# Kernel tuning notes

Hardware: AMD Instinct MI355X
Metric: run time of the kernel (lower is better)

Reference implementation:

```python
import jax, jax.numpy as jnp
import numpy as np

N = 50000   # nodes (subjects in population graph)
E = 800000  # edges (similarity graph, avg degree 16)
F = 128     # node features


def setup_inputs() -> dict:
    key = jax.random.key(0)
    ks = jax.random.split(key, 8)

    def glorot(k, shape):
        scale = 1.0 / np.sqrt(shape[0])
        return jax.random.normal(k, shape, jnp.float32) * scale

    x = jax.random.normal(ks[0], (N, F), jnp.float32)
    edge_index = jax.random.randint(ks[1], (2, E), 0, N, dtype=jnp.int64)
    return {
        "x": x,
        "edge_index": edge_index,
        "W1": glorot(ks[2], (F, 128)),   "b1": jnp.zeros((128,), jnp.float32),
        "W2": glorot(ks[3], (128, 64)),  "b2": jnp.zeros((64,), jnp.float32),
        "Wf1": glorot(ks[4], (64, 32)),  "bf1": jnp.zeros((32,), jnp.float32),
        "Wf2": glorot(ks[5], (32, 1)),   "bf2": jnp.zeros((1,), jnp.float32),
    }


def reference(x, edge_index, W1, b1, W2, b2, Wf1, bf1, Wf2, bf2):
    n = x.shape[0]
    # GCNConv (PyG default): add self-loops, symmetric deg^{-1/2} normalization
    loops = jnp.arange(n, dtype=edge_index.dtype)
    src = jnp.concatenate([edge_index[0], loops])  # [E+N]
    dst = jnp.concatenate([edge_index[1], loops])  # [E+N]
    deg = jax.ops.segment_sum(jnp.ones_like(dst, x.dtype), dst, num_segments=n)
    dinv = deg ** -0.5  # deg >= 1 thanks to self-loops
    norm = (dinv[src] * dinv[dst])[:, None]  # [E+N, 1]

    def gcn_conv(h, W, b):
        h = h @ W                                    # transform [n, out]
        msg = h[src] * norm                          # gather + normalize
        agg = jax.ops.segment_sum(msg, dst, num_segments=n)  # scatter-add
        return agg + b

    h = jnp.tanh(gcn_conv(x, W1, b1))
    h = jnp.tanh(gcn_conv(h, W2, b2))
    h = jnp.tanh(h @ Wf1 + bf1)
    return h @ Wf2 + bf2  # [n, 1] brain-age prediction
```

## Files before the change

kernel.cpp:

```cpp
#include <hip/hip_runtime.h>
#include <hip/hip_fp16.h>
#include <math.h>

#define TPB 256
#define CAP 64
#define BSHIFT 7
#define BSPAN 128
#define NBLK 256

typedef int   nt_i4 __attribute__((ext_vector_type(4)));
typedef unsigned nt_u4 __attribute__((ext_vector_type(4)));
typedef unsigned nt_u2 __attribute__((ext_vector_type(2)));

__global__ __launch_bounds__(TPB) void detect_dtype(const int* __restrict__ e,
                                                    int* __restrict__ flag) {
  __shared__ int found;
  if (threadIdx.x == 0) found = 0;
  __syncthreads();
  int nz = 0;
  for (int i = threadIdx.x; i < 2048; i += TPB)
    nz |= (e[2 * i + 1] != 0) ? 1 : 0;
  if (nz) atomicOr(&found, 1);
  __syncthreads();
  if (threadIdx.x == 0) *flag = found;
}

__device__ __forceinline__ void load_edge(const void* eptr, int flag, int E,
                                          int e, int& s, int& d) {
  if (flag) {
    const int* p = (const int*)eptr;
    s = p[e];
    d = p[E + e];
  } else {
    const long long* p = (const long long*)eptr;
    s = (int)p[e];
    d = (int)p[E + e];
  }
}

__global__ __launch_bounds__(TPB) void bucket_count(const void* __restrict__ eptr,
                                                    const int* __restrict__ flag,
                                                    int* __restrict__ cnt,
                                                    int E, int nbuck, int chunk) {
  extern __shared__ int hist[];
  const int tid = threadIdx.x;
  const int fl = *flag;
  for (int b = tid; b < nbuck; b += TPB) hist[b] = 0;
  __syncthreads();
  const int start = blockIdx.x * chunk;
  const int end = min(E, start + chunk);
  for (int e = start + tid; e < end; e += TPB) {
    int s, d;
    load_edge(eptr, fl, E, e, s, d);
    atomicAdd(&hist[d >> BSHIFT], 1);
  }
  __syncthreads();
  for (int b = tid; b < nbuck; b += TPB)
    cnt[blockIdx.x * nbuck + b] = hist[b];
}

__global__ __launch_bounds__(TPB) void scan_col(int* __restrict__ cnt,
                                                int* __restrict__ colsum,
                                                int nbuck) {
  __shared__ int buf[TPB];
  const int b = blockIdx.x;
  const int tid = threadIdx.x;
  int v = cnt[tid * nbuck + b];
  buf[tid] = v;
  __syncthreads();
  for (int off = 1; off < TPB; off <<= 1) {
    int t = (tid >= off) ? buf[tid - off] : 0;
    __syncthreads();
    buf[tid] += t;
    __syncthreads();
  }
  cnt[tid * nbuck + b] = buf[tid] - v;
  if (tid == TPB - 1) colsum[b] = buf[tid];
}

__global__ __launch_bounds__(TPB) void scan_bstart(const int* __restrict__ colsum,
                                                   int* __restrict__ bstart,
                                                   int nbuck, int E) {
  __shared__ int buf[TPB];
  __shared__ int carry;
  const int tid = threadIdx.x;
  if (tid == 0) carry = 0;
  __syncthreads();
  for (int base = 0; base < nbuck; base += TPB) {
    int i = base + tid;
    int v = (i < nbuck) ? colsum[i] : 0;
    buf[tid] = v;
    __syncthreads();
    for (int off = 1; off < TPB; off <<= 1) {
      int t = (tid >= off) ? buf[tid - off] : 0;
      __syncthreads();
      buf[tid] += t;
      __syncthreads();
    }
    if (i < nbuck) bstart[i] = carry + buf[tid] - v;
    __syncthreads();
    if (tid == TPB - 1) carry += buf[tid];
    __syncthreads();
  }
  if (tid == 0) bstart[nbuck] = E;
}

__global__ __launch_bounds__(TPB) void bucket_scatter(const void* __restrict__ eptr,
                                                      const int* __restrict__ flag,
                                                      const int* __restrict__ cnt,
                                                      const int* __restrict__ bstart,
                                                      unsigned long long* __restrict__ pairs,
                                                      int E, int nbuck, int chunk) {
  extern __shared__ int cur[];
  const int tid = threadIdx.x;
  const int fl = *flag;
  for (int b = tid; b < nbuck; b += TPB)
    cur[b] = bstart[b] + cnt[blockIdx.x * nbuck + b];
  __syncthreads();
  const int start = blockIdx.x * chunk;
  const int end = min(E, start + chunk);
  for (int e = start + tid; e < end; e += TPB) {
    int s, d;
    load_edge(eptr, fl, E, e, s, d);
    int slot = atomicAdd(&cur[d >> BSHIFT], 1);
    unsigned long long pv = ((unsigned long long)(unsigned)d << 32) | (unsigned)s;
    __builtin_nontemporal_store(pv, &pairs[slot]);
  }
}

__global__ __launch_bounds__(TPB) void ell_build(const unsigned long long* __restrict__ pairs,
                                                 const int* __restrict__ bstart,
                                                 int* __restrict__ ell,
                                                 int* __restrict__ degi,
                                                 float* __restrict__ dinv,
                                                 int n) {
  __shared__ int cnt[BSPAN];
  const int b = blockIdx.x;
  const int tid = threadIdx.x;
  const int base = b << BSHIFT;
  for (int j = tid; j < BSPAN; j += TPB) cnt[j] = 0;
  __syncthreads();
  const int start = bstart[b];
  const int end = bstart[b + 1];
  for (int i = start + tid; i < end; i += TPB) {
    unsigned long long pr = __builtin_nontemporal_load(&pairs[i]);
    int d = (int)(pr >> 32);
    int s = (int)(unsigned)pr;
    int slot = atomicAdd(&cnt[d - base], 1);
    if (slot < CAP) __builtin_nontemporal_store(s, &ell[(size_t)d * CAP + slot]);
  }
  __syncthreads();
  for (int j = tid; j < BSPAN; j += TPB) {
    int node = base + j;
    if (node < n) {
      int c = cnt[j];
      degi[node] = c;
      dinv[node] = rsqrtf((float)(c + 1));
    }
  }
}

template <int NC, typename AT>
__global__ __launch_bounds__(TPB, 4) void gemm_fast(const AT* __restrict__ A,
                                                    const float* __restrict__ W,
                                                    const float* __restrict__ dinv,
                                                    __half* __restrict__ out, int nrows) {
  constexpr int K = 128, TM = 64, BK = 32;
  constexpr int CPT = NC / 16;
  constexpr int AST = TM + 4;
  __shared__ float As[BK * AST];
  __shared__ float Ws[BK * NC];

  const int tid = threadIdx.x;
  const int tx = tid % 16;
  const int ty = tid / 16;
  const int r0 = ty * 4;
  const int block_row = blockIdx.x * TM;

  float acc[4][CPT];
#pragma unroll
  for (int r = 0; r < 4; r++)
#pragma unroll
    for (int c = 0; c < CPT; c++) acc[r][c] = 0.f;

  for (int k0 = 0; k0 < K; k0 += BK) {
#pragma unroll
    for (int i = 0; i < 2; i++) {
      int lid = tid + i * TPB;
      int r = lid / 8;
      int kk = (lid % 8) * 4;
      int gr = block_row + r;
      float4 v = make_float4(0.f, 0.f, 0.f, 0.f);
      if (gr < nrows) {
        if (sizeof(AT) == 4) {
          v = *(const float4*)&A[(size_t)gr * K + k0 + kk];
        } else {
          uint2 raw = *(const uint2*)&A[(size_t)gr * K + k0 + kk];
          const __half2* hh = (const __half2*)&raw;
          float2 f0 = __half22float2(hh[0]);
          float2 f1 = __half22float2(hh[1]);
          v = make_float4(f0.x, f0.y, f1.x, f1.y);
        }
      }
      As[(kk + 0) * AST + r] = v.x;
      As[(kk + 1) * AST + r] = v.y;
      As[(kk + 2) * AST + r] = v.z;
      As[(kk + 3) * AST + r] = v.w;
    }
#pragma unroll
    for (int i = 0; i < (BK * NC) / (4 * TPB); i++) {
      int lid = tid + i * TPB;
      int k = lid / (NC / 4);
      int c = (lid % (NC / 4)) * 4;
      *(float4*)&Ws[k * NC + c] = *(const float4*)&W[(size_t)(k0 + k) * NC + c];
    }
    __syncthreads();

#pragma unroll
    for (int k = 0; k < BK; k++) {
      float4 a = *(const float4*)&As[k * AST + r0];
      float av[4] = {a.x, a.y, a.z, a.w};
      float4 w0 = *(const float4*)&Ws[k * NC + tx * 4];
      float wv[CPT];
      wv[0] = w0.x; wv[1] = w0.y; wv[2] = w0.z; wv[3] = w0.w;
      if (NC == 128) {
        float4 w1 = *(const float4*)&Ws[k * NC + 64 + tx * 4];
        wv[4] = w1.x; wv[5] = w1.y; wv[6] = w1.z; wv[7] = w1.w;
      }
#pragma unroll
      for (int r = 0; r < 4; r++)
#pragma unroll
        for (int c = 0; c < CPT; c++) acc[r][c] += av[r] * wv[c];
    }
    __syncthreads();
  }

  union H4 { __half2 h[2]; uint2 u; };
#pragma unroll
  for (int r = 0; r < 4; r++) {
    int gr = block_row + r0 + r;
    if (gr >= nrows) continue;
    float di = dinv[gr];
    H4 p;
    p.h[0] = __float22half2_rn(make_float2(acc[r][0] * di, acc[r][1] * di));
    p.h[1] = __float22half2_rn(make_float2(acc[r][2] * di, acc[r][3] * di));
    *(uint2*)&out[(size_t)gr * NC + tx * 4] = p.u;
    if (NC == 128) {
      H4 q;
      q.h[0] = __float22half2_rn(make_float2(acc[r][4] * di, acc[r][5] * di));
      q.h[1] = __float22half2_rn(make_float2(acc[r][6] * di, acc[r][7] * di));
      *(uint2*)&out[(size_t)gr * NC + 64 + tx * 4] = q.u;
    }
  }
}

__global__ __launch_bounds__(TPB) void gcn_aggregate128(const int* __restrict__ degi,
                                                        const int* __restrict__ ell,
                                                        const __half* __restrict__ t,
                                                        const float* __restrict__ dinv,
                                                        const float* __restrict__ bias,
                                                        __half* __restrict__ h, int n) {
  constexpr int NC = 128, LPN = 16, CPL = 8, NPB = TPB / LPN;
  int tid = threadIdx.x;
  int node = blockIdx.x * NPB + tid / LPN;
  int lane = tid % LPN;
  if (node >= n) return;

  int deg = degi[node];
  if (deg > CAP) deg = CAP;
  const int* nbr = &ell[(size_t)node * CAP];
  const __half* tp = t + (size_t)lane * CPL;

  float acc[CPL];
#pragma unroll
  for (int c = 0; c < CPL; c++) acc[c] = 0.f;

  union Ld { uint4 u4; __half2 h[4]; };
  auto addv = [&](const Ld& v) {
#pragma unroll
    for (int c = 0; c < 4; c++) {
      float2 f = __half22float2(v.h[c]);
      acc[2 * c] += f.x;
      acc[2 * c + 1] += f.y;
    }
  };

  int j = 0;
  for (; j + 8 <= deg; j += 8) {
    nt_i4 n0 = __builtin_nontemporal_load((const nt_i4*)&nbr[j]);
    nt_i4 n1 = __builtin_nontemporal_load((const nt_i4*)&nbr[j + 4]);
    Ld v0, v1, v2, v3, v4, v5, v6, v7;
    v0.u4 = *(const uint4*)&tp[(size_t)n0.x * NC];
    v1.u4 = *(const uint4*)&tp[(size_t)n0.y * NC];
    v2.u4 = *(const uint4*)&tp[(size_t)n0.z * NC];
    v3.u4 = *(const uint4*)&tp[(size_t)n0.w * NC];
    v4.u4 = *(const uint4*)&tp[(size_t)n1.x * NC];
    v5.u4 = *(const uint4*)&tp[(size_t)n1.y * NC];
    v6.u4 = *(const uint4*)&tp[(size_t)n1.z * NC];
    v7.u4 = *(const uint4*)&tp[(size_t)n1.w * NC];
    addv(v0); addv(v1); addv(v2); addv(v3);
    addv(v4); addv(v5); addv(v6); addv(v7);
  }
  for (; j + 4 <= deg; j += 4) {
    nt_i4 n0 = __builtin_nontemporal_load((const nt_i4*)&nbr[j]);
    Ld v0, v1, v2, v3;
    v0.u4 = *(const uint4*)&tp[(size_t)n0.x * NC];
    v1.u4 = *(const uint4*)&tp[(size_t)n0.y * NC];
    v2.u4 = *(const uint4*)&tp[(size_t)n0.z * NC];
    v3.u4 = *(const uint4*)&tp[(size_t)n0.w * NC];
    addv(v0); addv(v1); addv(v2); addv(v3);
  }
  for (; j < deg; j++) {
    Ld v;
    v.u4 = *(const uint4*)&tp[(size_t)nbr[j] * NC];
    addv(v);
  }
  {
    Ld v;
    v.u4 = *(const uint4*)&tp[(size_t)node * NC];
    addv(v);
  }

  float di = dinv[node];
  const float* bp = &bias[lane * CPL];
  float bv[CPL];
#pragma unroll
  for (int c = 0; c < CPL; c += 4) {
    float4 b = *(const float4*)&bp[c];
    bv[c] = b.x; bv[c + 1] = b.y; bv[c + 2] = b.z; bv[c + 3] = b.w;
  }
  union { __half2 hh[4]; nt_u4 u; } o;
#pragma unroll
  for (int c = 0; c < CPL; c += 2)
    o.hh[c / 2] = __float22half2_rn(make_float2(tanhf(acc[c] * di + bv[c]),
                                                tanhf(acc[c + 1] * di + bv[c + 1])));
  __builtin_nontemporal_store(o.u, (nt_u4*)&h[(size_t)node * NC + lane * CPL]);
}

__global__ __launch_bounds__(TPB) void gcn_aggregate_head(
    const int* __restrict__ degi, const int* __restrict__ ell,
    const __half* __restrict__ t, const float* __restrict__ dinv,
    const float* __restrict__ b2, const float* __restrict__ Wf1,
    const float* __restrict__ bf1, const float* __restrict__ Wf2,
    const float* __restrict__ bf2, float* __restrict__ out, int n) {
  constexpr int NC = 64, LPN = 16, NPB = TPB / LPN;
  __shared__ float hrow[NPB][68];
  __shared__ float Wf1s[64 * 32];
  __shared__ float Wf2s[32];
  const int tid = threadIdx.x;

#pragma unroll
  for (int i = 0; i < 2; i++) {
    int lid = tid + i * TPB;
    *(float4*)&Wf1s[lid * 4] = *(const float4*)&Wf1[lid * 4];
  }
  if (tid < 32) Wf2s[tid] = Wf2[tid];

  const int g = tid / LPN;
  const int ll = tid % LPN;
  const int node = blockIdx.x * NPB + g;
  const bool active = node < n;

  float acc[4] = {0.f, 0.f, 0.f, 0.f};
  if (active) {
    int deg = degi[node];
    if (deg > CAP) deg = CAP;
    const int* nbr = &ell[(size_t)node * CAP];
    const __half* tp = t + (size_t)ll * 4;
    union Ld { uint2 u2; __half2 h[2]; };
    auto addv = [&](const Ld& v) {
      float2 f0 = __half22float2(v.h[0]);
      float2 f1 = __half22float2(v.h[1]);
      acc[0] += f0.x; acc[1] += f0.y; acc[2] += f1.x; acc[3] += f1.y;
    };
    int j = 0;
    for (; j + 4 <= deg; j += 4) {
      nt_i4 nn = __builtin_nontemporal_load((const nt_i4*)&nbr[j]);
      Ld v0, v1, v2, v3;
      v0.u2 = *(const uint2*)&tp[(size_t)nn.x * NC];
      v1.u2 = *(const uint2*)&tp[(size_t)nn.y * NC];
      v2.u2 = *(const uint2*)&tp[(size_t)nn.z * NC];
      v3.u2 = *(const uint2*)&tp[(size_t)nn.w * NC];
      addv(v0); addv(v1); addv(v2); addv(v3);
    }
    for (; j < deg; j++) {
      Ld v;
      v.u2 = *(const uint2*)&tp[(size_t)nbr[j] * NC];
      addv(v);
    }
    {
      Ld v;
      v.u2 = *(const uint2*)&tp[(size_t)node * NC];
      addv(v);
    }
    float di = dinv[node];
    float4 b = *(const float4*)&b2[ll * 4];
    hrow[g][ll * 4 + 0] = tanhf(acc[0] * di + b.x);
    hrow[g][ll * 4 + 1] = tanhf(acc[1] * di + b.y);
    hrow[g][ll * 4 + 2] = tanhf(acc[2] * di + b.z);
    hrow[g][ll * 4 + 3] = tanhf(acc[3] * di + b.w);
  }
  __syncthreads();

  float hid0 = bf1[ll];
  float hid1 = bf1[ll + 16];
#pragma unroll 8
  for (int i = 0; i < 64; i++) {
    float hv = hrow[g][i];
    hid0 += hv * Wf1s[i * 32 + ll];
    hid1 += hv * Wf1s[i * 32 + ll + 16];
  }
  float p = tanhf(hid0) * Wf2s[ll] + tanhf(hid1) * Wf2s[ll + 16];
  p += __shfl_down(p, 8, 16);
  p += __shfl_down(p, 4, 16);
  p += __shfl_down(p, 2, 16);
  p += __shfl_down(p, 1, 16);
  if (active && ll == 0) out[node] = p + bf2[0];
}

extern "C" void kernel_launch(void* const* d_in, const int* in_sizes, int n_in,
                              void* d_out, int out_size, void* d_ws, size_t ws_size,
                              hipStream_t stream) {
  const float* x   = (const float*)d_in[0];
  const void*  eix = d_in[1];
  const float* W1  = (const float*)d_in[2];
  const float* b1  = (const float*)d_in[3];
  const float* W2  = (const float*)d_in[4];
  const float* b2  = (const float*)d_in[5];
  const float* Wf1 = (const float*)d_in[6];
  const float* bf1 = (const float*)d_in[7];
  const float* Wf2 = (const float*)d_in[8];
  const float* bf2 = (const float*)d_in[9];
  float* out = (float*)d_out;

  const int N = in_sizes[0] / 128;
  const int E = in_sizes[1] / 2;
  const int nbuck = (N + BSPAN - 1) >> BSHIFT;
  const int chunk = (E + NBLK - 1) / NBLK;
  const size_t histBytes = (size_t)nbuck * 4;

  char* ws = (char*)d_ws;
  size_t off = 0;
  int* degi = (int*)(ws + off); off += (size_t)N * 4;
  float* dinv = (float*)(ws + off); off += (size_t)N * 4;
  int* flag = (int*)(ws + off); off += 64;
  int* cnt = (int*)(ws + off); off += (size_t)NBLK * nbuck * 4;
  int* colsum = (int*)(ws + off); off += (size_t)(nbuck + 4) * 4;
  int* bstart = (int*)(ws + off); off += (size_t)(nbuck + 4) * 4;
  off = (off + 15) & ~(size_t)15;
  unsigned long long* pairs = (unsigned long long*)(ws + off); off += (size_t)E * 8;
  int* ell = (int*)(ws + off); off += (size_t)N * CAP * 4;
  off = (off + 15) & ~(size_t)15;
  __half* t1 = (__half*)(ws + off); off += (size_t)N * 128 * 2;
  __half* h1 = (__half*)(ws + off); off += (size_t)N * 128 * 2;
  __half* t2 = t1;
  (void)ws_size; (void)n_in; (void)out_size;

  detect_dtype<<<1, TPB, 0, stream>>>((const int*)eix, flag);
  bucket_count<<<NBLK, TPB, histBytes, stream>>>(eix, flag, cnt, E, nbuck, chunk);
  scan_col<<<nbuck, TPB, 0, stream>>>(cnt, colsum, nbuck);
  scan_bstart<<<1, TPB, 0, stream>>>(colsum, bstart, nbuck, E);
  bucket_scatter<<<NBLK, TPB, histBytes, stream>>>(eix, flag, cnt, bstart, pairs, E, nbuck, chunk);
  ell_build<<<nbuck, TPB, 0, stream>>>(pairs, bstart, ell, degi, dinv, N);

  gemm_fast<128, float><<<(N + 63) / 64, TPB, 0, stream>>>(x, W1, dinv, t1, N);
  gcn_aggregate128<<<(N + 15) / 16, TPB, 0, stream>>>(degi, ell, t1, dinv, b1, h1, N);

  gemm_fast<64, __half><<<(N + 63) / 64, TPB, 0, stream>>>(h1, W2, dinv, t2, N);
  gcn_aggregate_head<<<(N + 15) / 16, TPB, 0, stream>>>(degi, ell, t2, dinv, b2,
                                                        Wf1, bf1, Wf2, bf2, out, N);
}
```

Measured before the change: 253.9 us.

## Replace FP32 SIMT GEMMs with FP16 MFMA 16x16x32 matrix-core kernels

Rewrites both dense transform GEMMs to use MFMA f16 instructions. W is converted to FP16 and stored transposed in shared memory, while A rows are loaded straight from global memory into registers, with FP32 x cast to FP16. The aim is to move the GEMM arithmetic from vector ALUs onto the matrix cores. In exchange, x is rounded to FP16 before the first multiply, and the output stores become scalar half writes instead of vectorized ones.

```diff
diff --git a/kernel.cpp b/kernel.cpp
--- a/kernel.cpp
+++ b/kernel.cpp
@@ -10,7 +10,8 @@
 
 typedef int   nt_i4 __attribute__((ext_vector_type(4)));
 typedef unsigned nt_u4 __attribute__((ext_vector_type(4)));
-typedef unsigned nt_u2 __attribute__((ext_vector_type(2)));
+typedef _Float16 f16x8 __attribute__((ext_vector_type(8)));
+typedef float f32x4 __attribute__((ext_vector_type(4)));
 
 __global__ __launch_bounds__(TPB) void detect_dtype(const int* __restrict__ e,
                                                     int* __restrict__ flag) {
@@ -161,96 +162,76 @@
 }
 
 template <int NC, typename AT>
-__global__ __launch_bounds__(TPB, 4) void gemm_fast(const AT* __restrict__ A,
+__global__ __launch_bounds__(TPB, 4) void gemm_mfma(const AT* __restrict__ A,
                                                     const float* __restrict__ W,
                                                     const float* __restrict__ dinv,
                                                     __half* __restrict__ out, int nrows) {
-  constexpr int K = 128, TM = 64, BK = 32;
-  constexpr int CPT = NC / 16;
-  constexpr int AST = TM + 4;
-  __shared__ float As[BK * AST];
-  __shared__ float Ws[BK * NC];
-
-  const int tid = threadIdx.x;
-  const int tx = tid % 16;
-  const int ty = tid / 16;
-  const int r0 = ty * 4;
-  const int block_row = blockIdx.x * TM;
-
-  float acc[4][CPT];
-#pragma unroll
-  for (int r = 0; r < 4; r++)
-#pragma unroll
-    for (int c = 0; c < CPT; c++) acc[r][c] = 0.f;
-
-  for (int k0 = 0; k0 < K; k0 += BK) {
-#pragma unroll
-    for (int i = 0; i < 2; i++) {
-      int lid = tid + i * TPB;
-      int r = lid / 8;
-      int kk = (lid % 8) * 4;
-      int gr = block_row + r;
-      float4 v = make_float4(0.f, 0.f, 0.f, 0.f);
-      if (gr < nrows) {
-        if (sizeof(AT) == 4) {
-          v = *(const float4*)&A[(size_t)gr * K + k0 + kk];
-        } else {
-          uint2 raw = *(const uint2*)&A[(size_t)gr * K + k0 + kk];
-          const __half2* hh = (const __half2*)&raw;
-          float2 f0 = __half22float2(hh[0]);
-          float2 f1 = __half22float2(hh[1]);
-          v = make_float4(f0.x, f0.y, f1.x, f1.y);
-        }
+  constexpr int K = 128;
+  constexpr int WT = 136;
+  constexpr int NT = NC / 16;
+  __shared__ _Float16 Wt[NC * WT];
+
+  const int tid = threadIdx.x;
+
+  for (int idx = tid; idx < NC * (K / 2); idx += TPB) {
+    int c = idx % NC;
+    int p = idx / NC;
+    float w0 = W[(2 * p) * NC + c];
+    float w1 = W[(2 * p + 1) * NC + c];
+    __half2* dst = (__half2*)&Wt[c * WT + 2 * p];
+    *dst = __floats2half2_rn(w0, w1);
+  }
+  __syncthreads();
+
+  const int w = tid >> 6;
+  const int lane = tid & 63;
+  const int l15 = lane & 15;
+  const int q = lane >> 4;
+  const int m_base = blockIdx.x * 64 + w * 16;
+  const int m = m_base + l15;
+  const bool mok = m < nrows;
+
+  f32x4 acc[NT];
+#pragma unroll
+  for (int t = 0; t < NT; t++) acc[t] = (f32x4){0.f, 0.f, 0.f, 0.f};
+
+#pragma unroll
+  for (int ks = 0; ks < 4; ks++) {
+    const int k0 = ks * 32;
+    f16x8 a;
+    if (sizeof(AT) == 4) {
+      float4 f0 = make_float4(0.f, 0.f, 0.f, 0.f), f1 = f0;
+      if (mok) {
+        const float* ap = (const float*)A + (size_t)m * K + k0 + q * 8;
+        f0 = *(const float4*)ap;
+        f1 = *(const float4*)(ap + 4);
       }
-      As[(kk + 0) * AST + r] = v.x;
-      As[(kk + 1) * AST + r] = v.y;
-      As[(kk + 2) * AST + r] = v.z;
-      As[(kk + 3) * AST + r] = v.w;
-    }
-#pragma unroll
-    for (int i = 0; i < (BK * NC) / (4 * TPB); i++) {
-      int lid = tid + i * TPB;
-      int k = lid / (NC / 4);
-      int c = (lid % (NC / 4)) * 4;
-      *(float4*)&Ws[k * NC + c] = *(const float4*)&W[(size_t)(k0 + k) * NC + c];
-    }
-    __syncthreads();
-
-#pragma unroll
-    for (int k = 0; k < BK; k++) {
-      float4 a = *(const float4*)&As[k * AST + r0];
-      float av[4] = {a.x, a.y, a.z, a.w};
-      float4 w0 = *(const float4*)&Ws[k * NC + tx * 4];
-      float wv[CPT];
-      wv[0] = w0.x; wv[1] = w0.y; wv[2] = w0.z; wv[3] = w0.w;
-      if (NC == 128) {
-        float4 w1 = *(const float4*)&Ws[k * NC + 64 + tx * 4];
-        wv[4] = w1.x; wv[5] = w1.y; wv[6] = w1.z; wv[7] = w1.w;
-      }
-#pragma unroll
-      for (int r = 0; r < 4; r++)
-#pragma unroll
-        for (int c = 0; c < CPT; c++) acc[r][c] += av[r] * wv[c];
-    }
-    __syncthreads();
-  }
-
-  union H4 { __half2 h[2]; uint2 u; };
+      a[0] = (_Float16)f0.x; a[1] = (_Float16)f0.y;
+      a[2] = (_Float16)f0.z; a[3] = (_Float16)f0.w;
+      a[4] = (_Float16)f1.x; a[5] = (_Float16)f1.y;
+      a[6] = (_Float16)f1.z; a[7] = (_Float16)f1.w;
+    } else {
+      union { uint4 u; f16x8 h; } ld;
+      ld.u = make_uint4(0, 0, 0, 0);
+      if (mok)
+        ld.u = *(const uint4*)((const __half*)A + (size_t)m * K + k0 + q * 8);
+      a = ld.h;
+    }
+#pragma unroll
+    for (int t = 0; t < NT; t++) {
+      f16x8 b = *(const f16x8*)&Wt[(t * 16 + l15) * WT + k0 + q * 8];
+      acc[t] = __builtin_amdgcn_mfma_f32_16x16x32_f16(a, b, acc[t], 0, 0, 0);
+    }
+  }
+
 #pragma unroll
   for (int r = 0; r < 4; r++) {
-    int gr = block_row + r0 + r;
-    if (gr >= nrows) continue;
-    float di = dinv[gr];
-    H4 p;
-    p.h[0] = __float22half2_rn(make_float2(acc[r][0] * di, acc[r][1] * di));
-    p.h[1] = __float22half2_rn(make_float2(acc[r][2] * di, acc[r][3] * di));
-    *(uint2*)&out[(size_t)gr * NC + tx * 4] = p.u;
-    if (NC == 128) {
-      H4 q;
-      q.h[0] = __float22half2_rn(make_float2(acc[r][4] * di, acc[r][5] * di));
-      q.h[1] = __float22half2_rn(make_float2(acc[r][6] * di, acc[r][7] * di));
-      *(uint2*)&out[(size_t)gr * NC + 64 + tx * 4] = q.u;
-    }
+    int row = m_base + q * 4 + r;
+    if (row >= nrows) continue;
+    float di = dinv[row];
+#pragma unroll
+    for (int t = 0; t < NT; t++)
+      out[(size_t)row * NC + t * 16 + l15] = (__half)(acc[t][r] * di);
   }
 }
 
@@ -463,10 +444,10 @@
   bucket_scatter<<<NBLK, TPB, histBytes, stream>>>(eix, flag, cnt, bstart, pairs, E, nbuck, chunk);
   ell_build<<<nbuck, TPB, 0, stream>>>(pairs, bstart, ell, degi, dinv, N);
 
-  gemm_fast<128, float><<<(N + 63) / 64, TPB, 0, stream>>>(x, W1, dinv, t1, N);
+  gemm_mfma<128, float><<<(N + 63) / 64, TPB, 0, stream>>>(x, W1, dinv, t1, N);
   gcn_aggregate128<<<(N + 15) / 16, TPB, 0, stream>>>(degi, ell, t1, dinv, b1, h1, N);
 
-  gemm_fast<64, __half><<<(N + 63) / 64, TPB, 0, stream>>>(h1, W2, dinv, t2, N);
+  gemm_mfma<64, __half><<<(N + 63) / 64, TPB, 0, stream>>>(h1, W2, dinv, t2, N);
   gcn_aggregate_head<<<(N + 15) / 16, TPB, 0, stream>>>(degi, ell, t2, dinv, b2,
                                                         Wf1, bf1, Wf2, bf2, out, N);
 }
```

After: 236.2 us. 1.08x faster.
